# Performance work log

Measured on AMD Instinct MI355X. Metric: run time of the kernel, lower is better.

## Reference

```python
import jax, jax.numpy as jnp
import numpy as np

PRIMES = [2, 3, 5, 7]  # from prime2idx {"2":0,"3":1,"5":2,"7":3}
NEG = float('-inf')


def setup_inputs() -> dict:
    B, O, T, P, L = 16384, 7, 64, 4, 7
    ks = jax.random.split(jax.random.key(0), 12)
    return {
        'program_seq': jax.random.randint(ks[0], (B, 20), 0, 7),
        'order_mask': jnp.zeros((B, O), jnp.float32),
        'tile_remain_budgets': jax.random.randint(ks[1], (B, L, P), 0, T),
        'tile_masks': jnp.zeros((B, L, P, T), jnp.float32),
        'cur_buffer_level': 1,
        'loop_ind': 2,
        'remain_buffer_size': jax.random.uniform(ks[2], (B,), jnp.float32, 1.0, 1e6),
        'tile2_max': jax.random.randint(ks[3], (B,), 32, T),
        'max_temporal_tile2': jax.random.uniform(ks[4], (B,), jnp.float32, 0.0, 10.0),
        'sp_tile2_max': jax.random.randint(ks[5], (B,), 16, 32),
        'sp_tile2_min': jax.random.randint(ks[6], (B,), 0, 8),
        'order_logit': jax.random.normal(ks[7], (B, O), jnp.float32),
        'tile_logits': jax.random.normal(ks[8], (B, P, T), jnp.float32),
        'sp_tile2_logit': jax.random.normal(ks[9], (B, T), jnp.float32),
    }


def _sample(key, score, mask):
    # categorical sample, its log-prob, and the 'more-than-one-option' mask
    action = jax.random.categorical(key, score)
    lp = jnp.take_along_axis(jax.nn.log_softmax(score, axis=-1), action[:, None], axis=1)[:, 0]
    lpm = ((mask == 0).sum(axis=-1) > 1).astype(score.dtype)
    return action, lp, lpm


def reference(program_seq, order_mask, tile_remain_budgets, tile_masks,
              cur_buffer_level, loop_ind, remain_buffer_size, tile2_max,
              max_temporal_tile2, sp_tile2_max, sp_tile2_min,
              order_logit, tile_logits, sp_tile2_logit):
    B = program_seq.shape[0]
    T = tile_masks.shape[-1]
    P = tile_logits.shape[1]
    n_levels = 3  # len(buffer_size_list)
    keys = jax.random.split(jax.random.key(1), 2 + P)
    j = jnp.arange(T)[None, :]  # [1,T] position grid for range masks

    # ---- order head ----
    order_score = order_logit + order_mask
    order_action, order_lp, order_lpm = _sample(keys[0], order_score, order_mask)

    if cur_buffer_level == n_levels:
        log_probs = jnp.zeros((B, 1 + P + 1), order_score.dtype).at[:, 0].set(order_lp)
        log_prob_masks = jnp.zeros((B, 1 + P + 1), order_score.dtype).at[:, 0].set(order_lpm)
        return order_action, None, None, log_probs, log_prob_masks

    tile2_base = tile_masks[:, loop_ind, 0]  # [B,T]

    # ---- spatial tile2: vectorized [min,max] range mask (replaces per-sample loops) ----
    sp_mask = jnp.where((j > sp_tile2_max[:, None]) | (j < sp_tile2_min[:, None]), NEG, tile2_base)
    sp_score = sp_tile2_logit + sp_mask
    sp_action, sp_lp, sp_lpm = _sample(keys[1], sp_score, sp_mask)

    # ---- temporal tile2 ----
    tile2_min = sp_action
    t2_max = jnp.minimum(tile2_max, tile2_min + max_temporal_tile2.astype(tile2_max.dtype))
    t2_mask = jnp.where((j > t2_max[:, None]) | (j < tile2_min[:, None]), NEG, tile2_base)
    t2_score = tile_logits[:, 0] + t2_mask
    tile2_action, t2_lp, t2_lpm = _sample(keys[2], t2_score, t2_mask)

    tile_actions = [tile2_action]
    sp_tile_actions = [sp_action]
    log_probs = [order_lp, t2_lp]
    log_prob_masks = [order_lpm, t2_lpm]

    tile_action = tile2_action
    rbs = remain_buffer_size
    for p in range(1, P):  # small fixed loop over primes
        rbs = rbs / jnp.power(jnp.float32(PRIMES[p - 1]), tile_action.astype(jnp.float32))
        tmax = jnp.log2(jnp.clip(rbs, 1.0)) / np.log2(PRIMES[p])
        tmax = jnp.clip(tmax.astype(jnp.int32), 0, T - 1)
        tmax = jnp.minimum(tmax, tile_remain_budgets[:, loop_ind, p].astype(jnp.int32))
        mask = jnp.where(j > tmax[:, None], NEG, tile_masks[:, loop_ind, p])
        score = tile_logits[:, p] + mask
        tile_action, lp, lpm = _sample(keys[2 + p], score, mask)
        tile_actions.append(tile_action)
        log_probs.append(lp)
        log_prob_masks.append(lpm)
        sp_tile_actions.append(jnp.zeros((B,), program_seq.dtype))

    log_probs.append(sp_lp)
    log_prob_masks.append(sp_lpm)

    return (order_action,
            jnp.stack(tile_actions, axis=1),
            jnp.stack(sp_tile_actions, axis=1),
            jnp.stack(log_probs, axis=1),
            jnp.stack(log_prob_masks, axis=1))
```

## Files before the change

### kernel.cpp

```cpp
#include <hip/hip_runtime.h>
#include <stdint.h>
#include <math.h>

__host__ __device__ static inline void tf2x32(uint32_t k0, uint32_t k1,
                                              uint32_t& x0, uint32_t& x1) {
  uint32_t ks2 = k0 ^ k1 ^ 0x1BD11BDAu;
  x0 += k0; x1 += k1;
#define TFR(r) { x0 += x1; x1 = (x1 << (r)) | (x1 >> (32 - (r))); x1 ^= x0; }
  TFR(13) TFR(15) TFR(26) TFR(6)
  x0 += k1;  x1 += ks2 + 1u;
  TFR(17) TFR(29) TFR(16) TFR(24)
  x0 += ks2; x1 += k0 + 2u;
  TFR(13) TFR(15) TFR(26) TFR(6)
  x0 += k0;  x1 += k1 + 3u;
  TFR(17) TFR(29) TFR(16) TFR(24)
  x0 += k1;  x1 += ks2 + 4u;
  TFR(13) TFR(15) TFR(26) TFR(6)
  x0 += ks2; x1 += k0 + 5u;
#undef TFR
}

struct Keys { uint32_t k[12]; };

struct SampleOut { int action; float lp; float lpm; };

struct DTab { double v[64]; };

constexpr double CEXP2(double w) {
  long i = (long)w;
  double f = w - (double)i;
  double y = f * 0.69314718055994530941723212145818;
  double term = 1.0, sum = 1.0;
  for (int k = 1; k <= 18; ++k) { term = term * y / (double)k; sum += term; }
  double p = 1.0;
  for (long k = 0; k < i; ++k) p *= 2.0;
  return sum * p;
}
constexpr DTab make_thresh(double l2p) {
  DTab t{};
  t.v[0] = 1e300;
  for (int k = 1; k < 64; ++k) t.v[k] = CEXP2((double)k * l2p);
  return t;
}
constexpr DTab make_invpw(int p) {
  DTab t{};
  double pw = 1.0;
  for (int k = 0; k < 64; ++k) { t.v[k] = 1.0 / pw; pw *= (double)p; }
  return t;
}
__constant__ DTab THR3 = make_thresh((double)1.5849625007211562f);
__constant__ DTab THR5 = make_thresh((double)2.321928094887362f);
__constant__ DTab THR7 = make_thresh((double)2.807354922057604f);
__constant__ DTab IPW2 = make_invpw(2);
__constant__ DTab IPW3 = make_invpw(3);
__constant__ DTab IPW5 = make_invpw(5);

template <int CTRL>
__device__ __forceinline__ float dpp_max_step(float v) {
  int o = __builtin_amdgcn_update_dpp(__float_as_int(v), __float_as_int(v),
                                      CTRL, 0xf, 0xf, false);
  return fmaxf(v, __int_as_float(o));
}
template <int CTRL>
__device__ __forceinline__ float dpp_add_step(float v) {
  int o = __builtin_amdgcn_update_dpp(0, __float_as_int(v),
                                      CTRL, 0xf, 0xf, false);
  return v + __int_as_float(o);
}
__device__ __forceinline__ float wave_max_bcast(float v) {
  v = dpp_max_step<0x111>(v);
  v = dpp_max_step<0x112>(v);
  v = dpp_max_step<0x114>(v);
  v = dpp_max_step<0x118>(v);
  v = dpp_max_step<0x142>(v);
  v = dpp_max_step<0x143>(v);
  return __int_as_float(__builtin_amdgcn_readlane(__float_as_int(v), 63));
}
__device__ __forceinline__ float wave_sum_bcast(float v) {
  v = dpp_add_step<0x111>(v);
  v = dpp_add_step<0x112>(v);
  v = dpp_add_step<0x114>(v);
  v = dpp_add_step<0x118>(v);
  v = dpp_add_step<0x142>(v);
  v = dpp_add_step<0x143>(v);
  return __int_as_float(__builtin_amdgcn_readlane(__float_as_int(v), 63));
}

__device__ __forceinline__ double readlane_d(double v, int lane) {
  union { double d; int i[2]; } u, r;
  u.d = v;
  r.i[0] = __builtin_amdgcn_readlane(u.i[0], lane);
  r.i[1] = __builtin_amdgcn_readlane(u.i[1], lane);
  return r.d;
}

__device__ static inline SampleOut sample_pre(float z, float es, float sc_full,
                                              bool lpm_pred) {
  float zmax = wave_max_bcast(z);
  unsigned long long ball = __ballot(z == zmax);
  int action = __builtin_amdgcn_readfirstlane(__ffsll(ball) - 1);
  float essum = wave_sum_bcast(es);
  float sa = __int_as_float(
      __builtin_amdgcn_readlane(__float_as_int(sc_full), action));
  unsigned long long mb = __ballot(lpm_pred);
  SampleOut r;
  r.action = action;
  r.lp = sa - logf(essum);
  r.lpm = (__popcll(mb) > 1) ? 1.0f : 0.0f;
  return r;
}

__device__ static inline float gumbel_f(uint32_t k0, uint32_t k1,
                                        uint32_t flat_idx) {
  uint32_t x0 = 0u, x1 = flat_idx;
  tf2x32(k0, k1, x0, x1);
  uint32_t bits = x0 ^ x1;
  uint32_t fb = (bits >> 9) | 0x3f800000u;
  float f = __uint_as_float(fb) - 1.0f;
  const float tinyf = 1.1754943508222875e-38f;
  float u = fmaxf(tinyf, f + tinyf);
  return -logf(-logf(u));
}

__global__ __launch_bounds__(256) void pt_kernel(
    const int*   __restrict__ loop_ind_p,
    const float* __restrict__ order_mask,
    const int*   __restrict__ tile_remain_budgets,
    const float* __restrict__ tile_masks,
    const float* __restrict__ remain_buffer_size,
    const int*   __restrict__ tile2_max,
    const float* __restrict__ max_temporal_tile2,
    const int*   __restrict__ sp_tile2_max,
    const int*   __restrict__ sp_tile2_min,
    const float* __restrict__ order_logit,
    const float* __restrict__ tile_logits,
    const float* __restrict__ sp_tile2_logit,
    float*       __restrict__ out,
    int B, int O, int T, int P, int L, Keys keys) {
  const int wave = threadIdx.x >> 6;
  const int t    = threadIdx.x & 63;
  const int b    = blockIdx.x * (blockDim.x >> 6) + wave;
  if (b >= B) return;

  const float NEGINF = -__builtin_inff();
  const int li = loop_ind_p[0];

  double thr3 = THR3.v[t], thr5 = THR5.v[t], thr7 = THR7.v[t];
  double ipw2 = IPW2.v[t], ipw3 = IPW3.v[t], ipw5 = IPW5.v[t];

  float g0 = gumbel_f(keys.k[0],  keys.k[1],  (uint32_t)(b * O + t));
  uint32_t fT = (uint32_t)(b * T + t);
  float g1 = gumbel_f(keys.k[2],  keys.k[3],  fT);
  float g2 = gumbel_f(keys.k[4],  keys.k[5],  fT);
  float g3 = gumbel_f(keys.k[6],  keys.k[7],  fT);
  float g4 = gumbel_f(keys.k[8],  keys.k[9],  fT);
  float g5 = gumbel_f(keys.k[10], keys.k[11], fT);

  float om  = (t < O) ? order_mask[(size_t)b * O + t] : 1.0f;
  float osc = (t < O) ? (order_logit[(size_t)b * O + t] + om) : NEGINF;

  const float* tm_row = tile_masks + ((size_t)b * L + li) * P * T;
  const float* tl_row = tile_logits + (size_t)b * P * T;
  float base0 = tm_row[t];
  float base1 = tm_row[T + t];
  float base2 = tm_row[2 * T + t];
  float base3 = tm_row[3 * T + t];

  int spmx = sp_tile2_max[b], spmn = sp_tile2_min[b];
  float spmask = (t > spmx || t < spmn) ? NEGINF : base0;
  float spsc   = sp_tile2_logit[(size_t)b * T + t] + spmask;

  float sc2f = tl_row[t]         + base0;
  float sc3f = tl_row[T + t]     + base1;
  float sc4f = tl_row[2 * T + t] + base2;
  float sc5f = tl_row[3 * T + t] + base3;
  float es2f = expf(sc2f), es3f = expf(sc3f);
  float es4f = expf(sc4f), es5f = expf(sc5f);
  float z2f = sc2f + g2, z3f = sc3f + g3, z4f = sc4f + g4, z5f = sc5f + g5;

  const int* budg = tile_remain_budgets + ((size_t)b * L + li) * P;
  int bu1 = budg[1], bu2 = budg[2], bu3 = budg[3];
  int t2maxcap = tile2_max[b];
  int mt = (int)max_temporal_tile2[b];
  float rbs = remain_buffer_size[b];

  SampleOut so = sample_pre(osc + g0, expf(osc), osc,
                            (t < O) && (om == 0.0f));

  SampleOut ssp = sample_pre(spsc + g1, expf(spsc), spsc, spmask == 0.0f);

  int t2min = ssp.action;
  int t2mx = min(t2maxcap, t2min + mt);
  bool pv2 = (t <= t2mx) && (t >= t2min);
  SampleOut st2 = sample_pre(pv2 ? z2f : NEGINF, pv2 ? es2f : 0.0f, sc2f,
                             pv2 && (base0 == 0.0f));

  int   pact[3];
  float plp[3], plpm[3];

  int prev = st2.action;
  {
    rbs = (float)((double)rbs * readlane_d(ipw2, prev));
    double x = (double)fmaxf(rbs, 1.0f);
    int tmax = min((int)__popcll(__ballot(x >= thr3)), bu1);
    bool pv = (t <= tmax);
    SampleOut s = sample_pre(pv ? z3f : NEGINF, pv ? es3f : 0.0f, sc3f,
                             pv && (base1 == 0.0f));
    pact[0] = s.action; plp[0] = s.lp; plpm[0] = s.lpm; prev = s.action;
  }
  {
    rbs = (float)((double)rbs * readlane_d(ipw3, prev));
    double x = (double)fmaxf(rbs, 1.0f);
    int tmax = min((int)__popcll(__ballot(x >= thr5)), bu2);
    bool pv = (t <= tmax);
    SampleOut s = sample_pre(pv ? z4f : NEGINF, pv ? es4f : 0.0f, sc4f,
                             pv && (base2 == 0.0f));
    pact[1] = s.action; plp[1] = s.lp; plpm[1] = s.lpm; prev = s.action;
  }
  {
    rbs = (float)((double)rbs * readlane_d(ipw5, prev));
    double x = (double)fmaxf(rbs, 1.0f);
    int tmax = min((int)__popcll(__ballot(x >= thr7)), bu3);
    bool pv = (t <= tmax);
    SampleOut s = sample_pre(pv ? z5f : NEGINF, pv ? es5f : 0.0f, sc5f,
                             pv && (base3 == 0.0f));
    pact[2] = s.action; plp[2] = s.lp; plpm[2] = s.lpm;
  }

  if (t == 0) {
    size_t Bz = (size_t)B;
    out[b] = (float)so.action;
    if (((B & 3) == 0)) {
      float4 ta4; ta4.x = (float)st2.action; ta4.y = (float)pact[0];
      ta4.z = (float)pact[1]; ta4.w = (float)pact[2];
      *(float4*)(out + Bz + (size_t)b * 4) = ta4;
      float4 sa4; sa4.x = (float)ssp.action; sa4.y = 0.0f;
      sa4.z = 0.0f; sa4.w = 0.0f;
      *(float4*)(out + Bz * 5 + (size_t)b * 4) = sa4;
      float* lp = out + Bz * 9 + (size_t)b * 6;
      float2 a, c, d;
      a.x = so.lp;  a.y = st2.lp;  *(float2*)(lp) = a;
      c.x = plp[0]; c.y = plp[1];  *(float2*)(lp + 2) = c;
      d.x = plp[2]; d.y = ssp.lp;  *(float2*)(lp + 4) = d;
      float* lm = out + Bz * 15 + (size_t)b * 6;
      a.x = so.lpm;  a.y = st2.lpm;  *(float2*)(lm) = a;
      c.x = plpm[0]; c.y = plpm[1];  *(float2*)(lm + 2) = c;
      d.x = plpm[2]; d.y = ssp.lpm;  *(float2*)(lm + 4) = d;
    } else {
      float* ta = out + Bz + (size_t)b * 4;
      ta[0] = (float)st2.action; ta[1] = (float)pact[0];
      ta[2] = (float)pact[1];    ta[3] = (float)pact[2];
      float* sa = out + Bz * 5 + (size_t)b * 4;
      sa[0] = (float)ssp.action; sa[1] = 0.0f; sa[2] = 0.0f; sa[3] = 0.0f;
      float* lp = out + Bz * 9 + (size_t)b * 6;
      lp[0] = so.lp; lp[1] = st2.lp; lp[2] = plp[0];
      lp[3] = plp[1]; lp[4] = plp[2]; lp[5] = ssp.lp;
      float* lm = out + Bz * 15 + (size_t)b * 6;
      lm[0] = so.lpm; lm[1] = st2.lpm; lm[2] = plpm[0];
      lm[3] = plpm[1]; lm[4] = plpm[2]; lm[5] = ssp.lpm;
    }
  }
}

extern "C" void kernel_launch(void* const* d_in, const int* in_sizes, int n_in,
                              void* d_out, int out_size, void* d_ws,
                              size_t ws_size, hipStream_t stream) {
  const int B = in_sizes[6];
  const int O = in_sizes[1] / B;
  const int T = in_sizes[13] / B;
  const int P = in_sizes[12] / (B * T);
  const int L = in_sizes[2] / (B * P);

  Keys keys;
  for (int j = 0; j < 6; ++j) {
    uint32_t x0 = 0u, x1 = (uint32_t)j;
    tf2x32(0u, 1u, x0, x1);
    keys.k[2 * j]     = x0;
    keys.k[2 * j + 1] = x1;
  }

  const int wavesPerBlock = 4;
  dim3 block(wavesPerBlock * 64);
  dim3 grid((B + wavesPerBlock - 1) / wavesPerBlock);
  pt_kernel<<<grid, block, 0, stream>>>(
      (const int*)d_in[5],
      (const float*)d_in[1],
      (const int*)d_in[2],
      (const float*)d_in[3],
      (const float*)d_in[6],
      (const int*)d_in[7],
      (const float*)d_in[8],
      (const int*)d_in[9],
      (const int*)d_in[10],
      (const float*)d_in[11],
      (const float*)d_in[12],
      (const float*)d_in[13],
      (float*)d_out, B, O, T, P, L, keys);
}
```

Measured before the change: 206.9 us.

## Precompute wave prefix max/sum so sequential prime stages need only readlanes

Computes wave-wide prefix max and prefix sum of the gumbel-perturbed scores and exponentials for each tile head before the dependent chain. Each prime stage then reads the max and the softmax denominator at lane tmax instead of running a full DPP reduction, which shortens the serial critical path. The tile2 head uses a prefix-sum difference over its range, the 7-wide order head uses a shortened 8-lane reduction, and logf/expf become the fast __logf/__expf intrinsics, which may change low-order bits. The fallback for B not divisible by 4 is dropped, and the prefix-sum difference can lose precision.

```diff
diff --git a/kernel.cpp b/kernel.cpp
--- a/kernel.cpp
+++ b/kernel.cpp
@@ -55,37 +55,60 @@
 __constant__ DTab IPW3 = make_invpw(3);
 __constant__ DTab IPW5 = make_invpw(5);
 
-template <int CTRL>
+#define NEGINF_I 0xff800000
+
+template <int CTRL, int RMASK>
 __device__ __forceinline__ float dpp_max_step(float v) {
-  int o = __builtin_amdgcn_update_dpp(__float_as_int(v), __float_as_int(v),
-                                      CTRL, 0xf, 0xf, false);
+  int o = __builtin_amdgcn_update_dpp((int)NEGINF_I, __float_as_int(v),
+                                      CTRL, RMASK, 0xf, false);
   return fmaxf(v, __int_as_float(o));
 }
-template <int CTRL>
+template <int CTRL, int RMASK>
 __device__ __forceinline__ float dpp_add_step(float v) {
   int o = __builtin_amdgcn_update_dpp(0, __float_as_int(v),
-                                      CTRL, 0xf, 0xf, false);
+                                      CTRL, RMASK, 0xf, false);
   return v + __int_as_float(o);
 }
 __device__ __forceinline__ float wave_max_bcast(float v) {
-  v = dpp_max_step<0x111>(v);
-  v = dpp_max_step<0x112>(v);
-  v = dpp_max_step<0x114>(v);
-  v = dpp_max_step<0x118>(v);
-  v = dpp_max_step<0x142>(v);
-  v = dpp_max_step<0x143>(v);
+  v = dpp_max_step<0x111, 0xf>(v);
+  v = dpp_max_step<0x112, 0xf>(v);
+  v = dpp_max_step<0x114, 0xf>(v);
+  v = dpp_max_step<0x118, 0xf>(v);
+  v = dpp_max_step<0x142, 0xf>(v);
+  v = dpp_max_step<0x143, 0xf>(v);
   return __int_as_float(__builtin_amdgcn_readlane(__float_as_int(v), 63));
 }
 __device__ __forceinline__ float wave_sum_bcast(float v) {
-  v = dpp_add_step<0x111>(v);
-  v = dpp_add_step<0x112>(v);
-  v = dpp_add_step<0x114>(v);
-  v = dpp_add_step<0x118>(v);
-  v = dpp_add_step<0x142>(v);
-  v = dpp_add_step<0x143>(v);
+  v = dpp_add_step<0x111, 0xf>(v);
+  v = dpp_add_step<0x112, 0xf>(v);
+  v = dpp_add_step<0x114, 0xf>(v);
+  v = dpp_add_step<0x118, 0xf>(v);
+  v = dpp_add_step<0x142, 0xf>(v);
+  v = dpp_add_step<0x143, 0xf>(v);
   return __int_as_float(__builtin_amdgcn_readlane(__float_as_int(v), 63));
 }
-
+__device__ __forceinline__ float wave_prefix_max(float v) {
+  v = dpp_max_step<0x111, 0xf>(v);
+  v = dpp_max_step<0x112, 0xf>(v);
+  v = dpp_max_step<0x114, 0xf>(v);
+  v = dpp_max_step<0x118, 0xf>(v);
+  v = dpp_max_step<0x142, 0xa>(v);
+  v = dpp_max_step<0x143, 0xc>(v);
+  return v;
+}
+__device__ __forceinline__ float wave_prefix_sum(float v) {
+  v = dpp_add_step<0x111, 0xf>(v);
+  v = dpp_add_step<0x112, 0xf>(v);
+  v = dpp_add_step<0x114, 0xf>(v);
+  v = dpp_add_step<0x118, 0xf>(v);
+  v = dpp_add_step<0x142, 0xa>(v);
+  v = dpp_add_step<0x143, 0xc>(v);
+  return v;
+}
+
+__device__ __forceinline__ float readlane_f(float v, int lane) {
+  return __int_as_float(__builtin_amdgcn_readlane(__float_as_int(v), lane));
+}
 __device__ __forceinline__ double readlane_d(double v, int lane) {
   union { double d; int i[2]; } u, r;
   u.d = v;
@@ -94,18 +117,17 @@
   return r.d;
 }
 
-__device__ static inline SampleOut sample_pre(float z, float es, float sc_full,
-                                              bool lpm_pred) {
+__device__ static inline SampleOut sample_full(float z, float es, float sc_full,
+                                               bool lpm_pred) {
   float zmax = wave_max_bcast(z);
   unsigned long long ball = __ballot(z == zmax);
   int action = __builtin_amdgcn_readfirstlane(__ffsll(ball) - 1);
   float essum = wave_sum_bcast(es);
-  float sa = __int_as_float(
-      __builtin_amdgcn_readlane(__float_as_int(sc_full), action));
+  float sa = readlane_f(sc_full, action);
   unsigned long long mb = __ballot(lpm_pred);
   SampleOut r;
   r.action = action;
-  r.lp = sa - logf(essum);
+  r.lp = sa - __logf(essum);
   r.lpm = (__popcll(mb) > 1) ? 1.0f : 0.0f;
   return r;
 }
@@ -119,7 +141,7 @@
   float f = __uint_as_float(fb) - 1.0f;
   const float tinyf = 1.1754943508222875e-38f;
   float u = fmaxf(tinyf, f + tinyf);
-  return -logf(-logf(u));
+  return -__logf(-__logf(u));
 }
 
 __global__ __launch_bounds__(256) void pt_kernel(
@@ -141,6 +163,7 @@
   const int t    = threadIdx.x & 63;
   const int b    = blockIdx.x * (blockDim.x >> 6) + wave;
   if (b >= B) return;
+  const int bs = __builtin_amdgcn_readfirstlane(b);
 
   const float NEGINF = -__builtin_inff();
   const int li = loop_ind_p[0];
@@ -148,117 +171,127 @@
   double thr3 = THR3.v[t], thr5 = THR5.v[t], thr7 = THR7.v[t];
   double ipw2 = IPW2.v[t], ipw3 = IPW3.v[t], ipw5 = IPW5.v[t];
 
-  float g0 = gumbel_f(keys.k[0],  keys.k[1],  (uint32_t)(b * O + t));
-  uint32_t fT = (uint32_t)(b * T + t);
+  float g0 = gumbel_f(keys.k[0],  keys.k[1],  (uint32_t)(bs * O + t));
+  uint32_t fT = (uint32_t)(bs * T + t);
   float g1 = gumbel_f(keys.k[2],  keys.k[3],  fT);
   float g2 = gumbel_f(keys.k[4],  keys.k[5],  fT);
   float g3 = gumbel_f(keys.k[6],  keys.k[7],  fT);
   float g4 = gumbel_f(keys.k[8],  keys.k[9],  fT);
   float g5 = gumbel_f(keys.k[10], keys.k[11], fT);
 
-  float om  = (t < O) ? order_mask[(size_t)b * O + t] : 1.0f;
-  float osc = (t < O) ? (order_logit[(size_t)b * O + t] + om) : NEGINF;
-
-  const float* tm_row = tile_masks + ((size_t)b * L + li) * P * T;
-  const float* tl_row = tile_logits + (size_t)b * P * T;
+  float om  = (t < O) ? order_mask[(size_t)bs * O + t] : 1.0f;
+  float osc = (t < O) ? (order_logit[(size_t)bs * O + t] + om) : NEGINF;
+
+  const float* tm_row = tile_masks + ((size_t)bs * L + li) * P * T;
+  const float* tl_row = tile_logits + (size_t)bs * P * T;
   float base0 = tm_row[t];
   float base1 = tm_row[T + t];
   float base2 = tm_row[2 * T + t];
   float base3 = tm_row[3 * T + t];
 
-  int spmx = sp_tile2_max[b], spmn = sp_tile2_min[b];
+  int spmx = sp_tile2_max[bs], spmn = sp_tile2_min[bs];
   float spmask = (t > spmx || t < spmn) ? NEGINF : base0;
-  float spsc   = sp_tile2_logit[(size_t)b * T + t] + spmask;
+  float spsc   = sp_tile2_logit[(size_t)bs * T + t] + spmask;
 
   float sc2f = tl_row[t]         + base0;
   float sc3f = tl_row[T + t]     + base1;
   float sc4f = tl_row[2 * T + t] + base2;
   float sc5f = tl_row[3 * T + t] + base3;
-  float es2f = expf(sc2f), es3f = expf(sc3f);
-  float es4f = expf(sc4f), es5f = expf(sc5f);
+  float es2f = __expf(sc2f), es3f = __expf(sc3f);
+  float es4f = __expf(sc4f), es5f = __expf(sc5f);
   float z2f = sc2f + g2, z3f = sc3f + g3, z4f = sc4f + g4, z5f = sc5f + g5;
 
-  const int* budg = tile_remain_budgets + ((size_t)b * L + li) * P;
+  float ps2 = wave_prefix_sum(es2f);
+  float pm3 = wave_prefix_max(z3f), ps3 = wave_prefix_sum(es3f);
+  float pm4 = wave_prefix_max(z4f), ps4 = wave_prefix_sum(es4f);
+  float pm5 = wave_prefix_max(z5f), ps5 = wave_prefix_sum(es5f);
+
+  const int* budg = tile_remain_budgets + ((size_t)bs * L + li) * P;
   int bu1 = budg[1], bu2 = budg[2], bu3 = budg[3];
-  int t2maxcap = tile2_max[b];
-  int mt = (int)max_temporal_tile2[b];
-  float rbs = remain_buffer_size[b];
-
-  SampleOut so = sample_pre(osc + g0, expf(osc), osc,
-                            (t < O) && (om == 0.0f));
-
-  SampleOut ssp = sample_pre(spsc + g1, expf(spsc), spsc, spmask == 0.0f);
-
-  int t2min = ssp.action;
-  int t2mx = min(t2maxcap, t2min + mt);
-  bool pv2 = (t <= t2mx) && (t >= t2min);
-  SampleOut st2 = sample_pre(pv2 ? z2f : NEGINF, pv2 ? es2f : 0.0f, sc2f,
-                             pv2 && (base0 == 0.0f));
+  int t2maxcap = tile2_max[bs];
+  int mt = (int)max_temporal_tile2[bs];
+  float rbs = remain_buffer_size[bs];
+
+  SampleOut so;
+  {
+    float z0 = osc + g0;
+    float es0 = __expf(osc);
+    float mv = z0, sv = es0;
+    mv = dpp_max_step<0x111, 0xf>(mv);
+    mv = dpp_max_step<0x112, 0xf>(mv);
+    mv = dpp_max_step<0x114, 0xf>(mv);
+    sv = dpp_add_step<0x111, 0xf>(sv);
+    sv = dpp_add_step<0x112, 0xf>(sv);
+    sv = dpp_add_step<0x114, 0xf>(sv);
+    float zmax = readlane_f(mv, 7);
+    unsigned long long ball = __ballot(z0 == zmax);
+    so.action = __builtin_amdgcn_readfirstlane(__ffsll(ball) - 1);
+    float essum = readlane_f(sv, 7);
+    so.lp = readlane_f(osc, so.action) - __logf(essum);
+    unsigned long long mb = __ballot((t < O) && (om == 0.0f));
+    so.lpm = (__popcll(mb) > 1) ? 1.0f : 0.0f;
+  }
+
+  SampleOut ssp = sample_full(spsc + g1, __expf(spsc), spsc, spmask == 0.0f);
+
+  SampleOut st2;
+  {
+    int t2min = ssp.action;
+    int t2mx = min(t2maxcap, t2min + mt);
+    bool pv2 = (t <= t2mx) && (t >= t2min);
+    float zm2 = pv2 ? z2f : NEGINF;
+    float zmax = wave_max_bcast(zm2);
+    unsigned long long ball = __ballot(zm2 == zmax);
+    st2.action = __builtin_amdgcn_readfirstlane(__ffsll(ball) - 1);
+    float hi = readlane_f(ps2, t2mx);
+    float lo = readlane_f(ps2, max(t2min - 1, 0));
+    float essum = hi - ((t2min > 0) ? lo : 0.0f);
+    st2.lp = readlane_f(sc2f, st2.action) - __logf(essum);
+    unsigned long long mb = __ballot(pv2 && (base0 == 0.0f));
+    st2.lpm = (__popcll(mb) > 1) ? 1.0f : 0.0f;
+  }
 
   int   pact[3];
   float plp[3], plpm[3];
-
   int prev = st2.action;
-  {
-    rbs = (float)((double)rbs * readlane_d(ipw2, prev));
-    double x = (double)fmaxf(rbs, 1.0f);
-    int tmax = min((int)__popcll(__ballot(x >= thr3)), bu1);
-    bool pv = (t <= tmax);
-    SampleOut s = sample_pre(pv ? z3f : NEGINF, pv ? es3f : 0.0f, sc3f,
-                             pv && (base1 == 0.0f));
-    pact[0] = s.action; plp[0] = s.lp; plpm[0] = s.lpm; prev = s.action;
-  }
-  {
-    rbs = (float)((double)rbs * readlane_d(ipw3, prev));
-    double x = (double)fmaxf(rbs, 1.0f);
-    int tmax = min((int)__popcll(__ballot(x >= thr5)), bu2);
-    bool pv = (t <= tmax);
-    SampleOut s = sample_pre(pv ? z4f : NEGINF, pv ? es4f : 0.0f, sc4f,
-                             pv && (base2 == 0.0f));
-    pact[1] = s.action; plp[1] = s.lp; plpm[1] = s.lpm; prev = s.action;
-  }
-  {
-    rbs = (float)((double)rbs * readlane_d(ipw5, prev));
-    double x = (double)fmaxf(rbs, 1.0f);
-    int tmax = min((int)__popcll(__ballot(x >= thr7)), bu3);
-    bool pv = (t <= tmax);
-    SampleOut s = sample_pre(pv ? z5f : NEGINF, pv ? es5f : 0.0f, sc5f,
-                             pv && (base3 == 0.0f));
-    pact[2] = s.action; plp[2] = s.lp; plpm[2] = s.lpm;
-  }
+#define P_STAGE(IDX, IPW, THR, BU, PM, PS, ZF, SCF, BASE)                    \
+  {                                                                          \
+    rbs = (float)((double)rbs * readlane_d(IPW, prev));                      \
+    double x = (double)fmaxf(rbs, 1.0f);                                     \
+    int tmax = min((int)__popcll(__ballot(x >= THR)), BU);                   \
+    float zmax = readlane_f(PM, tmax);                                       \
+    unsigned long long ball = __ballot((ZF == zmax) && (t <= tmax));         \
+    int act = __builtin_amdgcn_readfirstlane(__ffsll(ball) - 1);             \
+    float essum = readlane_f(PS, tmax);                                      \
+    pact[IDX] = act;                                                         \
+    plp[IDX]  = readlane_f(SCF, act) - __logf(essum);                        \
+    unsigned long long mb = __ballot((t <= tmax) && (BASE == 0.0f));         \
+    plpm[IDX] = (__popcll(mb) > 1) ? 1.0f : 0.0f;                            \
+    prev = act;                                                              \
+  }
+  P_STAGE(0, ipw2, thr3, bu1, pm3, ps3, z3f, sc3f, base1)
+  P_STAGE(1, ipw3, thr5, bu2, pm4, ps4, z4f, sc4f, base2)
+  P_STAGE(2, ipw5, thr7, bu3, pm5, ps5, z5f, sc5f, base3)
+#undef P_STAGE
 
   if (t == 0) {
     size_t Bz = (size_t)B;
     out[b] = (float)so.action;
-    if (((B & 3) == 0)) {
-      float4 ta4; ta4.x = (float)st2.action; ta4.y = (float)pact[0];
-      ta4.z = (float)pact[1]; ta4.w = (float)pact[2];
-      *(float4*)(out + Bz + (size_t)b * 4) = ta4;
-      float4 sa4; sa4.x = (float)ssp.action; sa4.y = 0.0f;
-      sa4.z = 0.0f; sa4.w = 0.0f;
-      *(float4*)(out + Bz * 5 + (size_t)b * 4) = sa4;
-      float* lp = out + Bz * 9 + (size_t)b * 6;
-      float2 a, c, d;
-      a.x = so.lp;  a.y = st2.lp;  *(float2*)(lp) = a;
-      c.x = plp[0]; c.y = plp[1];  *(float2*)(lp + 2) = c;
-      d.x = plp[2]; d.y = ssp.lp;  *(float2*)(lp + 4) = d;
-      float* lm = out + Bz * 15 + (size_t)b * 6;
-      a.x = so.lpm;  a.y = st2.lpm;  *(float2*)(lm) = a;
-      c.x = plpm[0]; c.y = plpm[1];  *(float2*)(lm + 2) = c;
-      d.x = plpm[2]; d.y = ssp.lpm;  *(float2*)(lm + 4) = d;
-    } else {
-      float* ta = out + Bz + (size_t)b * 4;
-      ta[0] = (float)st2.action; ta[1] = (float)pact[0];
-      ta[2] = (float)pact[1];    ta[3] = (float)pact[2];
-      float* sa = out + Bz * 5 + (size_t)b * 4;
-      sa[0] = (float)ssp.action; sa[1] = 0.0f; sa[2] = 0.0f; sa[3] = 0.0f;
-      float* lp = out + Bz * 9 + (size_t)b * 6;
-      lp[0] = so.lp; lp[1] = st2.lp; lp[2] = plp[0];
-      lp[3] = plp[1]; lp[4] = plp[2]; lp[5] = ssp.lp;
-      float* lm = out + Bz * 15 + (size_t)b * 6;
-      lm[0] = so.lpm; lm[1] = st2.lpm; lm[2] = plpm[0];
-      lm[3] = plpm[1]; lm[4] = plpm[2]; lm[5] = ssp.lpm;
-    }
+    float4 ta4; ta4.x = (float)st2.action; ta4.y = (float)pact[0];
+    ta4.z = (float)pact[1]; ta4.w = (float)pact[2];
+    *(float4*)(out + Bz + (size_t)b * 4) = ta4;
+    float4 sa4; sa4.x = (float)ssp.action; sa4.y = 0.0f;
+    sa4.z = 0.0f; sa4.w = 0.0f;
+    *(float4*)(out + Bz * 5 + (size_t)b * 4) = sa4;
+    float* lp = out + Bz * 9 + (size_t)b * 6;
+    float2 a, c, d;
+    a.x = so.lp;  a.y = st2.lp;  *(float2*)(lp) = a;
+    c.x = plp[0]; c.y = plp[1];  *(float2*)(lp + 2) = c;
+    d.x = plp[2]; d.y = ssp.lp;  *(float2*)(lp + 4) = d;
+    float* lm = out + Bz * 15 + (size_t)b * 6;
+    a.x = so.lpm;  a.y = st2.lpm;  *(float2*)(lm) = a;
+    c.x = plpm[0]; c.y = plpm[1];  *(float2*)(lm + 2) = c;
+    d.x = plpm[2]; d.y = ssp.lpm;  *(float2*)(lm + 4) = d;
   }
 }
 
```

Result: no change. 203.1 us (-1.8%).
